# Kernel optimization log

Hardware: AMD Instinct MI355X
Metric: run time of the kernel (lower is better)

The kernel has to match this reference:

```python
import jax, jax.numpy as jnp
import numpy as np

N = 50000   # num nodes
E = 800000  # num edges
D = 128     # embedding dim
EPS = 1e-5


def setup_inputs() -> dict:
    key = jax.random.key(0)
    ks = jax.random.split(key, 16)
    x = jnp.arange(N, dtype=jnp.int32)
    edge_index = jax.random.randint(ks[0], (2, E), 0, N, dtype=jnp.int32)
    weight = jax.random.uniform(ks[1], (E,), dtype=jnp.float32)
    emb = jax.random.normal(ks[2], (N, D), dtype=jnp.float32)
    # layer dims: 128->128, 128->64, 64->32
    dims = [(128, 128), (128, 64), (64, 32)]
    inp = {"x": x, "edge_index": edge_index, "weight": weight, "emb": emb}
    for i, (fi, fo) in enumerate(dims, start=1):
        s = 1.0 / np.sqrt(fi)
        inp[f"W{i}"] = jax.random.uniform(ks[3 * i], (fi, fo), dtype=jnp.float32, minval=-s, maxval=s)
        inp[f"b{i}"] = jnp.zeros((fo,), dtype=jnp.float32)
        inp[f"g{i}"] = jnp.ones((fo,), dtype=jnp.float32)
        inp[f"be{i}"] = jnp.zeros((fo,), dtype=jnp.float32)
    return inp


def _gcn_conv(h, src, dst, w, W, b):
    # PyG GCNConv: linear, add self-loops (weight 1), symmetric normalization, scatter-add
    h = h @ W  # [N, Fout]
    loop = jnp.arange(N, dtype=src.dtype)
    src_l = jnp.concatenate([src, loop])
    dst_l = jnp.concatenate([dst, loop])
    w_l = jnp.concatenate([w, jnp.ones((N,), w.dtype)])
    deg = jax.ops.segment_sum(w_l, dst_l, num_segments=N)
    dinv = jnp.where(deg > 0, jax.lax.rsqrt(jnp.maximum(deg, 1e-30)), 0.0)
    norm = dinv[src_l] * w_l * dinv[dst_l]  # [E+N]
    msg = h[src_l] * norm[:, None]          # gather + scale, [E+N, Fout]
    out = jax.ops.segment_sum(msg, dst_l, num_segments=N)
    return out + b


def _batch_norm(h, g, be):
    mu = h.mean(axis=0)
    var = h.var(axis=0)  # biased, as torch BN uses for normalization
    return (h - mu) * jax.lax.rsqrt(var + EPS) * g + be


def reference(x, edge_index, weight, emb,
              W1, b1, g1, be1,
              W2, b2, g2, be2,
              W3, b3, g3, be3):
    src, dst = edge_index[0], edge_index[1]
    h = emb[x]  # embedding lookup
    h = _batch_norm(_gcn_conv(h, src, dst, weight, W1, b1), g1, be1)
    h = jax.nn.relu(h)
    h = _batch_norm(_gcn_conv(h, src, dst, weight, W2, b2), g2, be2)
    h = jax.nn.relu(h)
    h = _batch_norm(_gcn_conv(h, src, dst, weight, W3, b3), g3, be3)
    return h
```

## Files before the change

kernel.cpp:

```cpp
#include <hip/hip_runtime.h>
#include <hip/hip_bf16.h>

#define BN_EPS 1e-5f
#define FIXSCALE 16777216.0f
#define FIXINV   5.9604644775390625e-08
#define LOWMASK  0xFFFFFFFFFFULL

typedef __attribute__((ext_vector_type(8))) short bf16x8;
typedef __attribute__((ext_vector_type(4))) float f32x4;

__device__ __forceinline__ unsigned short bfu(float v) {
  return __bfloat16_as_ushort(__float2bfloat16(v));
}
__device__ __forceinline__ unsigned int pk_bf2(float a, float b) {
  return (unsigned int)bfu(a) | ((unsigned int)bfu(b) << 16);
}
__device__ __forceinline__ float bf_lo(unsigned int u) { return __uint_as_float(u << 16); }
__device__ __forceinline__ float bf_hi(unsigned int u) { return __uint_as_float(u & 0xFFFF0000u); }


__global__ void zero_graph_k(unsigned long long* __restrict__ packed, int n) {
  int i = blockIdx.x * blockDim.x + threadIdx.x;
  if (i < n) packed[i] = 0ULL;
}

__global__ void hist64_k(const int* __restrict__ dst, const float* __restrict__ w,
                         unsigned long long* __restrict__ packed, int* __restrict__ rank, int e) {
  int i = blockIdx.x * blockDim.x + threadIdx.x;
  if (i < e) {
    unsigned long long fw = (unsigned long long)__float2uint_rn(w[i] * FIXSCALE);
    unsigned long long old = atomicAdd(&packed[dst[i]], (1ULL << 40) | fw);
    rank[i] = (int)(old >> 40);
  }
}

__global__ void scan_partial_k(const unsigned long long* __restrict__ packed,
                               int* __restrict__ bsum, float* __restrict__ dinv, int n) {
  __shared__ int s[256];
  int idx = blockIdx.x * 256 + threadIdx.x;
  unsigned long long p = (idx < n) ? packed[idx] : 0ULL;
  if (idx < n)
    dinv[idx] = rsqrtf(1.0f + (float)((double)(p & LOWMASK) * FIXINV));
  s[threadIdx.x] = (int)(p >> 40);
  __syncthreads();
  for (int off = 128; off > 0; off >>= 1) {
    if (threadIdx.x < off) s[threadIdx.x] += s[threadIdx.x + off];
    __syncthreads();
  }
  if (threadIdx.x == 0) bsum[blockIdx.x] = s[0];
}

__global__ void scan_tops_k(int* __restrict__ bsum, int* __restrict__ total_out, int nb) {
  __shared__ int s[256];
  int t = threadIdx.x;
  int v = (t < nb) ? bsum[t] : 0;
  s[t] = v;
  __syncthreads();
  for (int off = 1; off < 256; off <<= 1) {
    int u = (t >= off) ? s[t - off] : 0;
    __syncthreads();
    s[t] += u;
    __syncthreads();
  }
  if (t < nb) bsum[t] = s[t] - v;
  if (t == 255) *total_out = s[255];
}

__global__ void scan_final_k(const unsigned long long* __restrict__ packed,
                             const int* __restrict__ bsum, int* __restrict__ rowptr, int n) {
  __shared__ int s[256];
  int b = blockIdx.x, t = threadIdx.x;
  int idx = b * 256 + t;
  int v = (idx < n) ? (int)(packed[idx] >> 40) : 0;
  s[t] = v;
  __syncthreads();
  for (int off = 1; off < 256; off <<= 1) {
    int u = (t >= off) ? s[t - off] : 0;
    __syncthreads();
    s[t] += u;
    __syncthreads();
  }
  if (idx < n) rowptr[idx] = bsum[b] + s[t] - v;
}

__global__ void scatter_nb_k(const int* __restrict__ src, const int* __restrict__ dst,
                             const float* __restrict__ w, const int* __restrict__ rank,
                             const float* __restrict__ dinv, const int* __restrict__ rowptr,
                             int2* __restrict__ csr, int e) {
  int i = blockIdx.x * blockDim.x + threadIdx.x;
  if (i < e) {
    int d = dst[i], s = src[i];
    int pos = rowptr[d] + rank[i];
    float c = dinv[s] * w[i] * dinv[d];
    csr[pos] = make_int2(s, __float_as_int(c));
  }
}


__global__ void wtrans_k(const float* __restrict__ W1, const float* __restrict__ W2,
                         const float* __restrict__ W3, unsigned short* __restrict__ wt1,
                         unsigned short* __restrict__ wt2, unsigned short* __restrict__ wt3) {
  int idx = blockIdx.x * 256 + threadIdx.x;
  if (idx < 128 * 128) {
    int c = idx >> 7, k = idx & 127;
    wt1[idx] = bfu(W1[k * 128 + c]);
    return;
  }
  idx -= 128 * 128;
  if (idx < 128 * 64) {
    int c = idx >> 7, k = idx & 127;
    wt2[idx] = bfu(W2[k * 64 + c]);
    return;
  }
  idx -= 128 * 64;
  if (idx < 64 * 32) {
    int c = idx >> 6, k = idx & 63;
    wt3[idx] = bfu(W3[k * 32 + c]);
  }
}


template <int FIN, int FOUT, bool BNIN, bool GATHER>
__global__ __launch_bounds__(256) void gemm_mfma_k(
    const float* __restrict__ H, const int* __restrict__ xidx,
    const float* __restrict__ scale, const float* __restrict__ shift,
    const unsigned short* __restrict__ WtG, unsigned short* __restrict__ out, int n) {
  constexpr int C4 = FIN / 4;
  constexpr int ldH = FIN + 8;
  constexpr int ldW = FIN + 8;
  constexpr int ldC = FOUT + 4;
  constexpr int NCT = FOUT / 16;
  constexpr int NK = FIN / 32;
  constexpr int HT_SH = 64 * ldH;
  constexpr int WT_SH = FOUT * ldW;
  constexpr int STAGE_B = (HT_SH + WT_SH) * 2;
  constexpr int C_B = 64 * ldC * 4;
  constexpr int BYTES = STAGE_B > C_B ? STAGE_B : C_B;

  __shared__ __align__(16) char smem[BYTES];
  unsigned short* Ht = (unsigned short*)smem;
  unsigned short* Wt = (unsigned short*)smem + HT_SH;
  float* Cs = (float*)smem;

  const int t = threadIdx.x;
  const int r0 = blockIdx.x * 64;

  constexpr int NH = 64 * C4 / 256;
#pragma unroll
  for (int i = 0; i < NH; ++i) {
    int idx = t + 256 * i;
    int r = idx / C4, c4 = idx % C4;
    int gr = r0 + r;
    if (gr < n) {
      int srow = GATHER ? xidx[gr] : gr;
      float4 v = *(const float4*)(H + (size_t)srow * FIN + c4 * 4);
      if (BNIN) {
        float4 sc = *(const float4*)(scale + c4 * 4);
        float4 sh = *(const float4*)(shift + c4 * 4);
        v.x = fmaxf(v.x * sc.x + sh.x, 0.f);
        v.y = fmaxf(v.y * sc.y + sh.y, 0.f);
        v.z = fmaxf(v.z * sc.z + sh.z, 0.f);
        v.w = fmaxf(v.w * sc.w + sh.w, 0.f);
      }
      ushort4 p;
      p.x = bfu(v.x); p.y = bfu(v.y); p.z = bfu(v.z); p.w = bfu(v.w);
      *(ushort4*)&Ht[r * ldH + c4 * 4] = p;
    }
  }
  constexpr int NWU = FOUT * FIN / 8 / 256;
#pragma unroll
  for (int i = 0; i < NWU; ++i) {
    int idx = t + 256 * i;
    int wr = idx / (FIN / 8), w8 = idx % (FIN / 8);
    *(uint4*)&Wt[wr * ldW + w8 * 8] = *(const uint4*)&WtG[wr * FIN + w8 * 8];
  }
  __syncthreads();

  const int w = t >> 6;
  const int l = t & 63;
  const int l15 = l & 15;
  const int kg = l >> 4;
  const int arow = w * 16 + l15;

  f32x4 acc[NCT];
#pragma unroll
  for (int c = 0; c < NCT; ++c) acc[c] = (f32x4){0.f, 0.f, 0.f, 0.f};

#pragma unroll
  for (int kk = 0; kk < NK; ++kk) {
    bf16x8 a = *(const bf16x8*)&Ht[arow * ldH + kk * 32 + kg * 8];
#pragma unroll
    for (int c = 0; c < NCT; ++c) {
      bf16x8 b = *(const bf16x8*)&Wt[(c * 16 + l15) * ldW + kk * 32 + kg * 8];
      acc[c] = __builtin_amdgcn_mfma_f32_16x16x32_bf16(a, b, acc[c], 0, 0, 0);
    }
  }
  __syncthreads();

#pragma unroll
  for (int c = 0; c < NCT; ++c)
#pragma unroll
    for (int m = 0; m < 4; ++m)
      Cs[(w * 16 + kg * 4 + m) * ldC + c * 16 + l15] = acc[c][m];
  __syncthreads();

  constexpr int NU = 64 * FOUT / 8 / 256;
#pragma unroll
  for (int i = 0; i < NU; ++i) {
    int u = t + 256 * i;
    int r = u / (FOUT / 8), c8 = u % (FOUT / 8);
    int gr = r0 + r;
    if (gr < n) {
      const float* p = &Cs[r * ldC + c8 * 8];
      float4 v0 = *(const float4*)p;
      float4 v1 = *(const float4*)(p + 4);
      uint4 o;
      o.x = pk_bf2(v0.x, v0.y); o.y = pk_bf2(v0.z, v0.w);
      o.z = pk_bf2(v1.x, v1.y); o.w = pk_bf2(v1.z, v1.w);
      *(uint4*)&out[(size_t)gr * FOUT + c8 * 8] = o;
    }
  }
}


template <int FOUT>
__global__ void agg_csr_k(const unsigned short* __restrict__ hW, const int* __restrict__ rowptr,
                          const int2* __restrict__ csr, const float* __restrict__ dinv,
                          const float* __restrict__ b, float* __restrict__ agg, int n) {
  constexpr int TPR = FOUT / 8;
  int gid = blockIdx.x * blockDim.x + threadIdx.x;
  int row = gid / TPR, j = gid % TPR;
  if (row >= n) return;

  const float di = dinv[row];
  const float c0 = di * di;
  const uint4 hu = *(const uint4*)(hW + (size_t)row * FOUT + j * 8);
  const float4 bb0 = *(const float4*)(b + j * 8);
  const float4 bb1 = *(const float4*)(b + j * 8 + 4);
  float4 a0 = make_float4(bf_lo(hu.x) * c0 + bb0.x, bf_hi(hu.x) * c0 + bb0.y,
                          bf_lo(hu.y) * c0 + bb0.z, bf_hi(hu.y) * c0 + bb0.w);
  float4 a1 = make_float4(bf_lo(hu.z) * c0 + bb1.x, bf_hi(hu.z) * c0 + bb1.y,
                          bf_lo(hu.w) * c0 + bb1.z, bf_hi(hu.w) * c0 + bb1.w);

  const int e0 = rowptr[row], e1 = rowptr[row + 1];
  int ee = e0;
  for (; ee + 1 < e1; ee += 2) {
    const int2 ed0 = csr[ee];
    const int2 ed1 = csr[ee + 1];
    const float cc0 = __int_as_float(ed0.y);
    const float cc1 = __int_as_float(ed1.y);
    const uint4 u0 = *(const uint4*)(hW + (size_t)ed0.x * FOUT + j * 8);
    const uint4 u1 = *(const uint4*)(hW + (size_t)ed1.x * FOUT + j * 8);
    a0.x += bf_lo(u0.x) * cc0; a0.y += bf_hi(u0.x) * cc0;
    a0.z += bf_lo(u0.y) * cc0; a0.w += bf_hi(u0.y) * cc0;
    a1.x += bf_lo(u0.z) * cc0; a1.y += bf_hi(u0.z) * cc0;
    a1.z += bf_lo(u0.w) * cc0; a1.w += bf_hi(u0.w) * cc0;
    a0.x += bf_lo(u1.x) * cc1; a0.y += bf_hi(u1.x) * cc1;
    a0.z += bf_lo(u1.y) * cc1; a0.w += bf_hi(u1.y) * cc1;
    a1.x += bf_lo(u1.z) * cc1; a1.y += bf_hi(u1.z) * cc1;
    a1.z += bf_lo(u1.w) * cc1; a1.w += bf_hi(u1.w) * cc1;
  }
  if (ee < e1) {
    const int2 ed0 = csr[ee];
    const float cc0 = __int_as_float(ed0.y);
    const uint4 u0 = *(const uint4*)(hW + (size_t)ed0.x * FOUT + j * 8);
    a0.x += bf_lo(u0.x) * cc0; a0.y += bf_hi(u0.x) * cc0;
    a0.z += bf_lo(u0.y) * cc0; a0.w += bf_hi(u0.y) * cc0;
    a1.x += bf_lo(u0.z) * cc0; a1.y += bf_hi(u0.z) * cc0;
    a1.z += bf_lo(u0.w) * cc0; a1.w += bf_hi(u0.w) * cc0;
  }

  float* orow = agg + (size_t)row * FOUT + j * 8;
  *(float4*)(orow) = a0;
  *(float4*)(orow + 4) = a1;
}


template <int FOUT>
__global__ __launch_bounds__(256) void bn_stats_part_k(
    const float* __restrict__ h, float* __restrict__ psum, float* __restrict__ psq, int n) {
  constexpr int TPR = FOUT / 4;
  constexpr int RPB = 256 / TPR;
  const int t = threadIdx.x;
  const int j = t % TPR;
  const int rp = t / TPR;

  float sx = 0.f, sy = 0.f, sz = 0.f, sw = 0.f;
  float qx = 0.f, qy = 0.f, qz = 0.f, qw = 0.f;
  for (int r = blockIdx.x * RPB + rp; r < n; r += gridDim.x * RPB) {
    float4 v = *(const float4*)(h + (size_t)r * FOUT + j * 4);
    sx += v.x; sy += v.y; sz += v.z; sw += v.w;
    qx += v.x * v.x; qy += v.y * v.y; qz += v.z * v.z; qw += v.w * v.w;
  }

  __shared__ float4 ls[256];
  __shared__ float4 lq[256];
  ls[t] = make_float4(sx, sy, sz, sw);
  lq[t] = make_float4(qx, qy, qz, qw);
  __syncthreads();
#pragma unroll
  for (int off = RPB / 2; off > 0; off >>= 1) {
    if (rp < off) {
      float4 a = ls[t], b2 = ls[t + off * TPR];
      ls[t] = make_float4(a.x + b2.x, a.y + b2.y, a.z + b2.z, a.w + b2.w);
      float4 c = lq[t], d = lq[t + off * TPR];
      lq[t] = make_float4(c.x + d.x, c.y + d.y, c.z + d.z, c.w + d.w);
    }
    __syncthreads();
  }
  if (rp == 0) {
    *(float4*)&psum[(size_t)blockIdx.x * FOUT + j * 4] = ls[j];
    *(float4*)&psq[(size_t)blockIdx.x * FOUT + j * 4] = lq[j];
  }
}

template <int FOUT>
__global__ __launch_bounds__(256) void bn_finalize2_k(
    const float* __restrict__ psum, const float* __restrict__ psq,
    const float* __restrict__ g, const float* __restrict__ be,
    float* __restrict__ scale, float* __restrict__ shift, int nb, int n) {
  constexpr int TPR = FOUT / 4;
  constexpr int GR = 256 / TPR;
  const int t = threadIdx.x;
  const int j = t % TPR;
  const int gr = t / TPR;

  float4 s = make_float4(0.f, 0.f, 0.f, 0.f);
  float4 q = make_float4(0.f, 0.f, 0.f, 0.f);
  for (int b = gr; b < nb; b += GR) {
    float4 v = *(const float4*)&psum[(size_t)b * FOUT + j * 4];
    float4 u = *(const float4*)&psq[(size_t)b * FOUT + j * 4];
    s.x += v.x; s.y += v.y; s.z += v.z; s.w += v.w;
    q.x += u.x; q.y += u.y; q.z += u.z; q.w += u.w;
  }
  __shared__ float4 ls[256];
  __shared__ float4 lq[256];
  ls[t] = s;
  lq[t] = q;
  __syncthreads();
#pragma unroll
  for (int off = GR / 2; off > 0; off >>= 1) {
    if (gr < off) {
      float4 a = ls[t], b2 = ls[t + off * TPR];
      ls[t] = make_float4(a.x + b2.x, a.y + b2.y, a.z + b2.z, a.w + b2.w);
      float4 c = lq[t], d = lq[t + off * TPR];
      lq[t] = make_float4(c.x + d.x, c.y + d.y, c.z + d.z, c.w + d.w);
    }
    __syncthreads();
  }
  if (gr == 0) {
    float4 s4 = ls[j], q4 = lq[j];
    float inv_n = 1.0f / (float)n;
    float mu[4] = {s4.x * inv_n, s4.y * inv_n, s4.z * inv_n, s4.w * inv_n};
    float qq[4] = {q4.x, q4.y, q4.z, q4.w};
#pragma unroll
    for (int k = 0; k < 4; ++k) {
      int c = j * 4 + k;
      float var = qq[k] * inv_n - mu[k] * mu[k];
      float sc = g[c] * rsqrtf(var + BN_EPS);
      scale[c] = sc;
      shift[c] = be[c] - mu[k] * sc;
    }
  }
}

template <int FOUT, bool RELU>
__global__ void bn_apply_k(const float* __restrict__ in, const float* __restrict__ scale,
                           const float* __restrict__ shift, float* __restrict__ out, int n) {
  constexpr int TPR = FOUT / 4;
  int gid = blockIdx.x * blockDim.x + threadIdx.x;
  int row = gid / TPR, j = gid % TPR;
  if (row >= n) return;
  float4 v = *(const float4*)(in + (size_t)row * FOUT + j * 4);
  float4 sc = *(const float4*)(scale + j * 4);
  float4 sh = *(const float4*)(shift + j * 4);
  float4 o;
  o.x = v.x * sc.x + sh.x;
  o.y = v.y * sc.y + sh.y;
  o.z = v.z * sc.z + sh.z;
  o.w = v.w * sc.w + sh.w;
  if (RELU) {
    o.x = fmaxf(o.x, 0.f);
    o.y = fmaxf(o.y, 0.f);
    o.z = fmaxf(o.z, 0.f);
    o.w = fmaxf(o.w, 0.f);
  }
  *(float4*)(out + (size_t)row * FOUT + j * 4) = o;
}


static inline size_t pad4(size_t v) { return (v + 3) & ~(size_t)3; }

extern "C" void kernel_launch(void* const* d_in, const int* in_sizes, int n_in,
                              void* d_out, int out_size, void* d_ws, size_t ws_size,
                              hipStream_t stream) {
  const int* x = (const int*)d_in[0];
  const int* ei = (const int*)d_in[1];
  const float* w = (const float*)d_in[2];
  const float* emb = (const float*)d_in[3];
  const float* W1 = (const float*)d_in[4];
  const float* b1 = (const float*)d_in[5];
  const float* g1 = (const float*)d_in[6];
  const float* be1 = (const float*)d_in[7];
  const float* W2 = (const float*)d_in[8];
  const float* b2 = (const float*)d_in[9];
  const float* g2 = (const float*)d_in[10];
  const float* be2 = (const float*)d_in[11];
  const float* W3 = (const float*)d_in[12];
  const float* b3 = (const float*)d_in[13];
  const float* g3 = (const float*)d_in[14];
  const float* be3 = (const float*)d_in[15];

  const int n = in_sizes[0];
  const int e = in_sizes[2];
  const int* src = ei;
  const int* dst = ei + e;

  float* ws = (float*)d_ws;
  size_t off = 0;
  unsigned short* bufA16 = (unsigned short*)(ws + off); off += pad4((size_t)n * 64);
  float* bufB = ws + off; off += pad4((size_t)n * 128);
  unsigned long long* packed = (unsigned long long*)(ws + off); off += pad4((size_t)n * 2);
  float* dinv = ws + off; off += pad4(n);
  int* rowptr = (int*)(ws + off); off += pad4(n + 1);
  int* rank = (int*)(ws + off); off += pad4(e);
  int2* csr = (int2*)(ws + off); off += pad4((size_t)e * 2);
  unsigned short* wt1 = (unsigned short*)(ws + off); off += 128 * 128 / 2;
  unsigned short* wt2 = (unsigned short*)(ws + off); off += 128 * 64 / 2;
  unsigned short* wt3 = (unsigned short*)(ws + off); off += 64 * 32 / 2;
  float* psum = ws + off; off += 256 * 128;
  float* psq = ws + off; off += 256 * 128;
  float* scale = ws + off; off += 128;
  float* shift = ws + off; off += 128;
  int* bsum = (int*)(ws + off); off += 256;

  const int B = 256;
  dim3 blk(B);
  const int nb = (n + 255) / 256;
  const int SB = 256;

  wtrans_k<<<(128 * 128 + 128 * 64 + 64 * 32 + B - 1) / B, blk, 0, stream>>>(W1, W2, W3, wt1, wt2, wt3);

  zero_graph_k<<<(n + B - 1) / B, blk, 0, stream>>>(packed, n);
  hist64_k<<<(e + B - 1) / B, blk, 0, stream>>>(dst, w, packed, rank, e);
  scan_partial_k<<<nb, blk, 0, stream>>>(packed, bsum, dinv, n);
  scan_tops_k<<<1, blk, 0, stream>>>(bsum, rowptr + n, nb);
  scan_final_k<<<nb, blk, 0, stream>>>(packed, bsum, rowptr, n);
  scatter_nb_k<<<(e + B - 1) / B, blk, 0, stream>>>(src, dst, w, rank, dinv, rowptr, csr, e);

  const int gx = (n + 63) / 64;

  gemm_mfma_k<128, 128, false, true><<<gx, blk, 0, stream>>>(emb, x, nullptr, nullptr, wt1, bufA16, n);
  agg_csr_k<128><<<((size_t)n * 16 + B - 1) / B, blk, 0, stream>>>(bufA16, rowptr, csr, dinv, b1, bufB, n);
  bn_stats_part_k<128><<<SB, blk, 0, stream>>>(bufB, psum, psq, n);
  bn_finalize2_k<128><<<1, blk, 0, stream>>>(psum, psq, g1, be1, scale, shift, SB, n);

  gemm_mfma_k<128, 64, true, false><<<gx, blk, 0, stream>>>(bufB, nullptr, scale, shift, wt2, bufA16, n);
  agg_csr_k<64><<<((size_t)n * 8 + B - 1) / B, blk, 0, stream>>>(bufA16, rowptr, csr, dinv, b2, bufB, n);
  bn_stats_part_k<64><<<SB, blk, 0, stream>>>(bufB, psum, psq, n);
  bn_finalize2_k<64><<<1, blk, 0, stream>>>(psum, psq, g2, be2, scale, shift, SB, n);

  gemm_mfma_k<64, 32, true, false><<<gx, blk, 0, stream>>>(bufB, nullptr, scale, shift, wt3, bufA16, n);
  agg_csr_k<32><<<((size_t)n * 4 + B - 1) / B, blk, 0, stream>>>(bufA16, rowptr, csr, dinv, b3, bufB, n);
  bn_stats_part_k<32><<<SB, blk, 0, stream>>>(bufB, psum, psq, n);
  bn_finalize2_k<32><<<1, blk, 0, stream>>>(psum, psq, g3, be3, scale, shift, SB, n);
  bn_apply_k<32, false><<<((size_t)n * 8 + B - 1) / B, blk, 0, stream>>>(bufB, scale, shift, (float*)d_out, n);
}
```

Measured before the change: 214.2 us.

## Store aggregated activations in bf16, tile layer-1 features per XCD, fuse prep kernels

```diff
diff --git a/kernel.cpp b/kernel.cpp
--- a/kernel.cpp
+++ b/kernel.cpp
@@ -18,11 +18,40 @@
 __device__ __forceinline__ float bf_lo(unsigned int u) { return __uint_as_float(u << 16); }
 __device__ __forceinline__ float bf_hi(unsigned int u) { return __uint_as_float(u & 0xFFFF0000u); }
 
-
-__global__ void zero_graph_k(unsigned long long* __restrict__ packed, int n) {
-  int i = blockIdx.x * blockDim.x + threadIdx.x;
-  if (i < n) packed[i] = 0ULL;
-}
+__device__ __forceinline__ void fma8(float* a, uint4 u, float c) {
+  a[0] += bf_lo(u.x) * c; a[1] += bf_hi(u.x) * c;
+  a[2] += bf_lo(u.y) * c; a[3] += bf_hi(u.y) * c;
+  a[4] += bf_lo(u.z) * c; a[5] += bf_hi(u.z) * c;
+  a[6] += bf_lo(u.w) * c; a[7] += bf_hi(u.w) * c;
+}
+
+__device__ __forceinline__ float4 load4(const float* p) { return *(const float4*)p; }
+__device__ __forceinline__ float4 load4(const unsigned short* p) {
+  uint2 u = *(const uint2*)p;
+  return make_float4(bf_lo(u.x), bf_hi(u.x), bf_lo(u.y), bf_hi(u.y));
+}
+
+
+__global__ void prep_k(const float* __restrict__ W1, const float* __restrict__ W2,
+                       const float* __restrict__ W3, unsigned short* __restrict__ wt1,
+                       unsigned short* __restrict__ wt2, unsigned short* __restrict__ wt3,
+                       unsigned long long* __restrict__ packed, int n) {
+  int idx = blockIdx.x * 256 + threadIdx.x;
+  if (idx < n) packed[idx] = 0ULL;
+  if (idx < 128 * 128) {
+    int c = idx >> 7, k = idx & 127;
+    wt1[idx] = bfu(W1[k * 128 + c]);
+  } else if (idx < 128 * 128 + 128 * 64) {
+    int i2 = idx - 128 * 128;
+    int c = i2 >> 7, k = i2 & 127;
+    wt2[i2] = bfu(W2[k * 64 + c]);
+  } else if (idx < 128 * 128 + 128 * 64 + 64 * 32) {
+    int i2 = idx - 128 * 128 - 128 * 64;
+    int c = i2 >> 6, k = i2 & 63;
+    wt3[i2] = bfu(W3[k * 32 + c]);
+  }
+}
+
 
 __global__ void hist64_k(const int* __restrict__ dst, const float* __restrict__ w,
                          unsigned long long* __restrict__ packed, int* __restrict__ rank, int e) {
@@ -97,32 +126,9 @@
 }
 
 
-__global__ void wtrans_k(const float* __restrict__ W1, const float* __restrict__ W2,
-                         const float* __restrict__ W3, unsigned short* __restrict__ wt1,
-                         unsigned short* __restrict__ wt2, unsigned short* __restrict__ wt3) {
-  int idx = blockIdx.x * 256 + threadIdx.x;
-  if (idx < 128 * 128) {
-    int c = idx >> 7, k = idx & 127;
-    wt1[idx] = bfu(W1[k * 128 + c]);
-    return;
-  }
-  idx -= 128 * 128;
-  if (idx < 128 * 64) {
-    int c = idx >> 7, k = idx & 127;
-    wt2[idx] = bfu(W2[k * 64 + c]);
-    return;
-  }
-  idx -= 128 * 64;
-  if (idx < 64 * 32) {
-    int c = idx >> 6, k = idx & 63;
-    wt3[idx] = bfu(W3[k * 32 + c]);
-  }
-}
-
-
-template <int FIN, int FOUT, bool BNIN, bool GATHER>
+template <typename TIN, int FIN, int FOUT, bool BNIN, bool GATHER, bool TILEOUT>
 __global__ __launch_bounds__(256) void gemm_mfma_k(
-    const float* __restrict__ H, const int* __restrict__ xidx,
+    const TIN* __restrict__ H, const int* __restrict__ xidx,
     const float* __restrict__ scale, const float* __restrict__ shift,
     const unsigned short* __restrict__ WtG, unsigned short* __restrict__ out, int n) {
   constexpr int C4 = FIN / 4;
@@ -153,7 +159,7 @@
     int gr = r0 + r;
     if (gr < n) {
       int srow = GATHER ? xidx[gr] : gr;
-      float4 v = *(const float4*)(H + (size_t)srow * FIN + c4 * 4);
+      float4 v = load4(H + (size_t)srow * FIN + c4 * 4);
       if (BNIN) {
         float4 sc = *(const float4*)(scale + c4 * 4);
         float4 sh = *(const float4*)(shift + c4 * 4);
@@ -217,16 +223,69 @@
       uint4 o;
       o.x = pk_bf2(v0.x, v0.y); o.y = pk_bf2(v0.z, v0.w);
       o.z = pk_bf2(v1.x, v1.y); o.w = pk_bf2(v1.z, v1.w);
-      *(uint4*)&out[(size_t)gr * FOUT + c8 * 8] = o;
+      if (TILEOUT) {
+        *(uint4*)&out[((size_t)(c8 >> 2) * n + gr) * 32 + (c8 & 3) * 8] = o;
+      } else {
+        *(uint4*)&out[(size_t)gr * FOUT + c8 * 8] = o;
+      }
     }
   }
+}
+
+
+__global__ __launch_bounds__(256) void agg_csr_t_k(
+    const unsigned short* __restrict__ hWt, const int* __restrict__ rowptr,
+    const int2* __restrict__ csr, const float* __restrict__ dinv,
+    const float* __restrict__ b, unsigned short* __restrict__ out, int n) {
+  const int bid = blockIdx.x;
+  const int xcd = bid & 7;
+  const int tile = xcd >> 1;
+  const int row0 = (bid >> 3) * 128 + (xcd & 1) * 64;
+  const int t = threadIdx.x;
+  const int j = t & 3;
+  const int row = row0 + (t >> 2);
+  if (row >= n) return;
+
+  const unsigned short* base = hWt + (size_t)tile * n * 32;
+  const float di = dinv[row];
+  const float c0 = di * di;
+  float a[8];
+  {
+    uint4 hu = *(const uint4*)(base + (size_t)row * 32 + j * 8);
+    const float4 bb0 = *(const float4*)(b + tile * 32 + j * 8);
+    const float4 bb1 = *(const float4*)(b + tile * 32 + j * 8 + 4);
+    a[0] = bb0.x; a[1] = bb0.y; a[2] = bb0.z; a[3] = bb0.w;
+    a[4] = bb1.x; a[5] = bb1.y; a[6] = bb1.z; a[7] = bb1.w;
+    fma8(a, hu, c0);
+  }
+
+  const int e0 = rowptr[row], e1 = rowptr[row + 1];
+  int ee = e0;
+  for (; ee + 1 < e1; ee += 2) {
+    const int2 d0 = csr[ee];
+    const int2 d1 = csr[ee + 1];
+    const uint4 u0 = *(const uint4*)(base + (size_t)d0.x * 32 + j * 8);
+    const uint4 u1 = *(const uint4*)(base + (size_t)d1.x * 32 + j * 8);
+    fma8(a, u0, __int_as_float(d0.y));
+    fma8(a, u1, __int_as_float(d1.y));
+  }
+  if (ee < e1) {
+    const int2 d0 = csr[ee];
+    const uint4 u0 = *(const uint4*)(base + (size_t)d0.x * 32 + j * 8);
+    fma8(a, u0, __int_as_float(d0.y));
+  }
+
+  uint4 o;
+  o.x = pk_bf2(a[0], a[1]); o.y = pk_bf2(a[2], a[3]);
+  o.z = pk_bf2(a[4], a[5]); o.w = pk_bf2(a[6], a[7]);
+  *(uint4*)&out[(size_t)row * 128 + tile * 32 + j * 8] = o;
 }
 
 
 template <int FOUT>
 __global__ void agg_csr_k(const unsigned short* __restrict__ hW, const int* __restrict__ rowptr,
                           const int2* __restrict__ csr, const float* __restrict__ dinv,
-                          const float* __restrict__ b, float* __restrict__ agg, int n) {
+                          const float* __restrict__ b, unsigned short* __restrict__ out, int n) {
   constexpr int TPR = FOUT / 8;
   int gid = blockIdx.x * blockDim.x + threadIdx.x;
   int row = gid / TPR, j = gid % TPR;
@@ -234,83 +293,82 @@
 
   const float di = dinv[row];
   const float c0 = di * di;
-  const uint4 hu = *(const uint4*)(hW + (size_t)row * FOUT + j * 8);
-  const float4 bb0 = *(const float4*)(b + j * 8);
-  const float4 bb1 = *(const float4*)(b + j * 8 + 4);
-  float4 a0 = make_float4(bf_lo(hu.x) * c0 + bb0.x, bf_hi(hu.x) * c0 + bb0.y,
-                          bf_lo(hu.y) * c0 + bb0.z, bf_hi(hu.y) * c0 + bb0.w);
-  float4 a1 = make_float4(bf_lo(hu.z) * c0 + bb1.x, bf_hi(hu.z) * c0 + bb1.y,
-                          bf_lo(hu.w) * c0 + bb1.z, bf_hi(hu.w) * c0 + bb1.w);
+  float a[8];
+  {
+    uint4 hu = *(const uint4*)(hW + (size_t)row * FOUT + j * 8);
+    const float4 bb0 = *(const float4*)(b + j * 8);
+    const float4 bb1 = *(const float4*)(b + j * 8 + 4);
+    a[0] = bb0.x; a[1] = bb0.y; a[2] = bb0.z; a[3] = bb0.w;
+    a[4] = bb1.x; a[5] = bb1.y; a[6] = bb1.z; a[7] = bb1.w;
+    fma8(a, hu, c0);
+  }
 
   const int e0 = rowptr[row], e1 = rowptr[row + 1];
   int ee = e0;
   for (; ee + 1 < e1; ee += 2) {
-    const int2 ed0 = csr[ee];
-    const int2 ed1 = csr[ee + 1];
-    const float cc0 = __int_as_float(ed0.y);
-    const float cc1 = __int_as_float(ed1.y);
-    const uint4 u0 = *(const uint4*)(hW + (size_t)ed0.x * FOUT + j * 8);
-    const uint4 u1 = *(const uint4*)(hW + (size_t)ed1.x * FOUT + j * 8);
-    a0.x += bf_lo(u0.x) * cc0; a0.y += bf_hi(u0.x) * cc0;
-    a0.z += bf_lo(u0.y) * cc0; a0.w += bf_hi(u0.y) * cc0;
-    a1.x += bf_lo(u0.z) * cc0; a1.y += bf_hi(u0.z) * cc0;
-    a1.z += bf_lo(u0.w) * cc0; a1.w += bf_hi(u0.w) * cc0;
-    a0.x += bf_lo(u1.x) * cc1; a0.y += bf_hi(u1.x) * cc1;
-    a0.z += bf_lo(u1.y) * cc1; a0.w += bf_hi(u1.y) * cc1;
-    a1.x += bf_lo(u1.z) * cc1; a1.y += bf_hi(u1.z) * cc1;
-    a1.z += bf_lo(u1.w) * cc1; a1.w += bf_hi(u1.w) * cc1;
+    const int2 d0 = csr[ee];
+    const int2 d1 = csr[ee + 1];
+    const uint4 u0 = *(const uint4*)(hW + (size_t)d0.x * FOUT + j * 8);
+    const uint4 u1 = *(const uint4*)(hW + (size_t)d1.x * FOUT + j * 8);
+    fma8(a, u0, __int_as_float(d0.y));
+    fma8(a, u1, __int_as_float(d1.y));
   }
   if (ee < e1) {
-    const int2 ed0 = csr[ee];
-    const float cc0 = __int_as_float(ed0.y);
-    const uint4 u0 = *(const uint4*)(hW + (size_t)ed0.x * FOUT + j * 8);
-    a0.x += bf_lo(u0.x) * cc0; a0.y += bf_hi(u0.x) * cc0;
-    a0.z += bf_lo(u0.y) * cc0; a0.w += bf_hi(u0.y) * cc0;
-    a1.x += bf_lo(u0.z) * cc0; a1.y += bf_hi(u0.z) * cc0;
-    a1.z += bf_lo(u0.w) * cc0; a1.w += bf_hi(u0.w) * cc0;
-  }
-
-  float* orow = agg + (size_t)row * FOUT + j * 8;
-  *(float4*)(orow) = a0;
-  *(float4*)(orow + 4) = a1;
+    const int2 d0 = csr[ee];
+    const uint4 u0 = *(const uint4*)(hW + (size_t)d0.x * FOUT + j * 8);
+    fma8(a, u0, __int_as_float(d0.y));
+  }
+
+  uint4 o;
+  o.x = pk_bf2(a[0], a[1]); o.y = pk_bf2(a[2], a[3]);
+  o.z = pk_bf2(a[4], a[5]); o.w = pk_bf2(a[6], a[7]);
+  *(uint4*)&out[(size_t)row * FOUT + j * 8] = o;
 }
 
 
 template <int FOUT>
 __global__ __launch_bounds__(256) void bn_stats_part_k(
-    const float* __restrict__ h, float* __restrict__ psum, float* __restrict__ psq, int n) {
-  constexpr int TPR = FOUT / 4;
+    const unsigned short* __restrict__ h, float* __restrict__ psum,
+    float* __restrict__ psq, int n) {
+  constexpr int TPR = FOUT / 8;
   constexpr int RPB = 256 / TPR;
   const int t = threadIdx.x;
   const int j = t % TPR;
   const int rp = t / TPR;
 
-  float sx = 0.f, sy = 0.f, sz = 0.f, sw = 0.f;
-  float qx = 0.f, qy = 0.f, qz = 0.f, qw = 0.f;
+  float s[8] = {0.f, 0.f, 0.f, 0.f, 0.f, 0.f, 0.f, 0.f};
+  float q[8] = {0.f, 0.f, 0.f, 0.f, 0.f, 0.f, 0.f, 0.f};
   for (int r = blockIdx.x * RPB + rp; r < n; r += gridDim.x * RPB) {
-    float4 v = *(const float4*)(h + (size_t)r * FOUT + j * 4);
-    sx += v.x; sy += v.y; sz += v.z; sw += v.w;
-    qx += v.x * v.x; qy += v.y * v.y; qz += v.z * v.z; qw += v.w * v.w;
-  }
-
-  __shared__ float4 ls[256];
-  __shared__ float4 lq[256];
-  ls[t] = make_float4(sx, sy, sz, sw);
-  lq[t] = make_float4(qx, qy, qz, qw);
+    uint4 u = *(const uint4*)(h + (size_t)r * FOUT + j * 8);
+    float v[8] = {bf_lo(u.x), bf_hi(u.x), bf_lo(u.y), bf_hi(u.y),
+                  bf_lo(u.z), bf_hi(u.z), bf_lo(u.w), bf_hi(u.w)};
+#pragma unroll
+    for (int k = 0; k < 8; ++k) { s[k] += v[k]; q[k] += v[k] * v[k]; }
+  }
+
+  __shared__ float4 ls0[256], ls1[256], lq0[256], lq1[256];
+  ls0[t] = make_float4(s[0], s[1], s[2], s[3]);
+  ls1[t] = make_float4(s[4], s[5], s[6], s[7]);
+  lq0[t] = make_float4(q[0], q[1], q[2], q[3]);
+  lq1[t] = make_float4(q[4], q[5], q[6], q[7]);
   __syncthreads();
 #pragma unroll
   for (int off = RPB / 2; off > 0; off >>= 1) {
     if (rp < off) {
-      float4 a = ls[t], b2 = ls[t + off * TPR];
-      ls[t] = make_float4(a.x + b2.x, a.y + b2.y, a.z + b2.z, a.w + b2.w);
-      float4 c = lq[t], d = lq[t + off * TPR];
-      lq[t] = make_float4(c.x + d.x, c.y + d.y, c.z + d.z, c.w + d.w);
+      int o = off * TPR;
+      float4 a, b2;
+      a = ls0[t]; b2 = ls0[t + o]; ls0[t] = make_float4(a.x + b2.x, a.y + b2.y, a.z + b2.z, a.w + b2.w);
+      a = ls1[t]; b2 = ls1[t + o]; ls1[t] = make_float4(a.x + b2.x, a.y + b2.y, a.z + b2.z, a.w + b2.w);
+      a = lq0[t]; b2 = lq0[t + o]; lq0[t] = make_float4(a.x + b2.x, a.y + b2.y, a.z + b2.z, a.w + b2.w);
+      a = lq1[t]; b2 = lq1[t + o]; lq1[t] = make_float4(a.x + b2.x, a.y + b2.y, a.z + b2.z, a.w + b2.w);
     }
     __syncthreads();
   }
   if (rp == 0) {
-    *(float4*)&psum[(size_t)blockIdx.x * FOUT + j * 4] = ls[j];
-    *(float4*)&psq[(size_t)blockIdx.x * FOUT + j * 4] = lq[j];
+    *(float4*)&psum[(size_t)blockIdx.x * FOUT + j * 8] = ls0[j];
+    *(float4*)&psum[(size_t)blockIdx.x * FOUT + j * 8 + 4] = ls1[j];
+    *(float4*)&psq[(size_t)blockIdx.x * FOUT + j * 8] = lq0[j];
+    *(float4*)&psq[(size_t)blockIdx.x * FOUT + j * 8 + 4] = lq1[j];
   }
 }
 
@@ -364,28 +422,26 @@
   }
 }
 
-template <int FOUT, bool RELU>
-__global__ void bn_apply_k(const float* __restrict__ in, const float* __restrict__ scale,
-                           const float* __restrict__ shift, float* __restrict__ out, int n) {
-  constexpr int TPR = FOUT / 4;
+__global__ void bn_apply32_k(const unsigned short* __restrict__ in,
+                             const float* __restrict__ scale, const float* __restrict__ shift,
+                             float* __restrict__ out, int n) {
   int gid = blockIdx.x * blockDim.x + threadIdx.x;
-  int row = gid / TPR, j = gid % TPR;
+  int row = gid >> 2, j = gid & 3;
   if (row >= n) return;
-  float4 v = *(const float4*)(in + (size_t)row * FOUT + j * 4);
-  float4 sc = *(const float4*)(scale + j * 4);
-  float4 sh = *(const float4*)(shift + j * 4);
-  float4 o;
-  o.x = v.x * sc.x + sh.x;
-  o.y = v.y * sc.y + sh.y;
-  o.z = v.z * sc.z + sh.z;
-  o.w = v.w * sc.w + sh.w;
-  if (RELU) {
-    o.x = fmaxf(o.x, 0.f);
-    o.y = fmaxf(o.y, 0.f);
-    o.z = fmaxf(o.z, 0.f);
-    o.w = fmaxf(o.w, 0.f);
-  }
-  *(float4*)(out + (size_t)row * FOUT + j * 4) = o;
+  uint4 u = *(const uint4*)(in + (size_t)row * 32 + j * 8);
+  float v[8] = {bf_lo(u.x), bf_hi(u.x), bf_lo(u.y), bf_hi(u.y),
+                bf_lo(u.z), bf_hi(u.z), bf_lo(u.w), bf_hi(u.w)};
+  const float4 sc0 = *(const float4*)(scale + j * 8);
+  const float4 sc1 = *(const float4*)(scale + j * 8 + 4);
+  const float4 sh0 = *(const float4*)(shift + j * 8);
+  const float4 sh1 = *(const float4*)(shift + j * 8 + 4);
+  float4 o0 = make_float4(v[0] * sc0.x + sh0.x, v[1] * sc0.y + sh0.y,
+                          v[2] * sc0.z + sh0.z, v[3] * sc0.w + sh0.w);
+  float4 o1 = make_float4(v[4] * sc1.x + sh1.x, v[5] * sc1.y + sh1.y,
+                          v[6] * sc1.z + sh1.z, v[7] * sc1.w + sh1.w);
+  float* p = out + (size_t)row * 32 + j * 8;
+  *(float4*)p = o0;
+  *(float4*)(p + 4) = o1;
 }
 
 
@@ -419,7 +475,7 @@
   float* ws = (float*)d_ws;
   size_t off = 0;
   unsigned short* bufA16 = (unsigned short*)(ws + off); off += pad4((size_t)n * 64);
-  float* bufB = ws + off; off += pad4((size_t)n * 128);
+  unsigned short* bufB16 = (unsigned short*)(ws + off); off += pad4((size_t)n * 64);
   unsigned long long* packed = (unsigned long long*)(ws + off); off += pad4((size_t)n * 2);
   float* dinv = ws + off; off += pad4(n);
   int* rowptr = (int*)(ws + off); off += pad4(n + 1);
@@ -439,9 +495,7 @@
   const int nb = (n + 255) / 256;
   const int SB = 256;
 
-  wtrans_k<<<(128 * 128 + 128 * 64 + 64 * 32 + B - 1) / B, blk, 0, stream>>>(W1, W2, W3, wt1, wt2, wt3);
-
-  zero_graph_k<<<(n + B - 1) / B, blk, 0, stream>>>(packed, n);
+  prep_k<<<(n + B - 1) / B, blk, 0, stream>>>(W1, W2, W3, wt1, wt2, wt3, packed, n);
   hist64_k<<<(e + B - 1) / B, blk, 0, stream>>>(dst, w, packed, rank, e);
   scan_partial_k<<<nb, blk, 0, stream>>>(packed, bsum, dinv, n);
   scan_tops_k<<<1, blk, 0, stream>>>(bsum, rowptr + n, nb);
@@ -450,19 +504,19 @@
 
   const int gx = (n + 63) / 64;
 
-  gemm_mfma_k<128, 128, false, true><<<gx, blk, 0, stream>>>(emb, x, nullptr, nullptr, wt1, bufA16, n);
-  agg_csr_k<128><<<((size_t)n * 16 + B - 1) / B, blk, 0, stream>>>(bufA16, rowptr, csr, dinv, b1, bufB, n);
-  bn_stats_part_k<128><<<SB, blk, 0, stream>>>(bufB, psum, psq, n);
+  gemm_mfma_k<float, 128, 128, false, true, true><<<gx, blk, 0, stream>>>(emb, x, nullptr, nullptr, wt1, bufA16, n);
+  agg_csr_t_k<<<((n + 127) / 128) * 8, blk, 0, stream>>>(bufA16, rowptr, csr, dinv, b1, bufB16, n);
+  bn_stats_part_k<128><<<SB, blk, 0, stream>>>(bufB16, psum, psq, n);
   bn_finalize2_k<128><<<1, blk, 0, stream>>>(psum, psq, g1, be1, scale, shift, SB, n);
 
-  gemm_mfma_k<128, 64, true, false><<<gx, blk, 0, stream>>>(bufB, nullptr, scale, shift, wt2, bufA16, n);
-  agg_csr_k<64><<<((size_t)n * 8 + B - 1) / B, blk, 0, stream>>>(bufA16, rowptr, csr, dinv, b2, bufB, n);
-  bn_stats_part_k<64><<<SB, blk, 0, stream>>>(bufB, psum, psq, n);
+  gemm_mfma_k<unsigned short, 128, 64, true, false, false><<<gx, blk, 0, stream>>>(bufB16, nullptr, scale, shift, wt2, bufA16, n);
+  agg_csr_k<64><<<((size_t)n * 8 + B - 1) / B, blk, 0, stream>>>(bufA16, rowptr, csr, dinv, b2, bufB16, n);
+  bn_stats_part_k<64><<<SB, blk, 0, stream>>>(bufB16, psum, psq, n);
   bn_finalize2_k<64><<<1, blk, 0, stream>>>(psum, psq, g2, be2, scale, shift, SB, n);
 
-  gemm_mfma_k<64, 32, true, false><<<gx, blk, 0, stream>>>(bufB, nullptr, scale, shift, wt3, bufA16, n);
-  agg_csr_k<32><<<((size_t)n * 4 + B - 1) / B, blk, 0, stream>>>(bufA16, rowptr, csr, dinv, b3, bufB, n);
-  bn_stats_part_k<32><<<SB, blk, 0, stream>>>(bufB, psum, psq, n);
+  gemm_mfma_k<unsigned short, 64, 32, true, false, false><<<gx, blk, 0, stream>>>(bufB16, nullptr, scale, shift, wt3, bufA16, n);
+  agg_csr_k<32><<<((size_t)n * 4 + B - 1) / B, blk, 0, stream>>>(bufA16, rowptr, csr, dinv, b3, bufB16, n);
+  bn_stats_part_k<32><<<SB, blk, 0, stream>>>(bufB16, psum, psq, n);
   bn_finalize2_k<32><<<1, blk, 0, stream>>>(psum, psq, g3, be3, scale, shift, SB, n);
-  bn_apply_k<32, false><<<((size_t)n * 8 + B - 1) / B, blk, 0, stream>>>(bufB, scale, shift, (float*)d_out, n);
-}
+  bn_apply32_k<<<((size_t)n * 4 + B - 1) / B, blk, 0, stream>>>(bufB16, scale, shift, (float*)d_out, n);
+}
```

Measured after the change: 213.9 us. No clear change (-0.2%).
